# Kernel tuning notes

Hardware: AMD Instinct MI355X
Metric: run time of the kernel (lower is better)

The kernel has to match this reference:

```python
import jax, jax.numpy as jnp
import numpy as np

CHUNK = 128  # chunk size for the chunked causal linear-attention scan
EPS = 1e-6


def _feature_map(x):
    # elu(x) + 1, matching torch.nn.functional.elu (alpha=1)
    return jax.nn.elu(x) + 1.0


def _causal_linear(Q, K, V):
    """Chunked causal linear attention.

    Q, K: [N, H, L, D], V: [N, H, L, Dv] (float32).
    Computes out[l] = Q[l] @ sum_{s<=l} K[s]^T V[s] without materializing
    the O(L*D*Dv) cumulative outer-product tensor.
    """
    N, H, L, D = Q.shape
    Dv = V.shape[-1]
    C = L // CHUNK
    # [C, N, H, T, D]
    qc = jnp.moveaxis(Q.reshape(N, H, C, CHUNK, D), 2, 0)
    kc = jnp.moveaxis(K.reshape(N, H, C, CHUNK, D), 2, 0)
    vc = jnp.moveaxis(V.reshape(N, H, C, CHUNK, Dv), 2, 0)
    tri = jnp.tril(jnp.ones((CHUNK, CHUNK), dtype=Q.dtype))  # causal mask within chunk

    def step(S, qkv):
        q, k, v = qkv  # [N, H, T, D], [N, H, T, D], [N, H, T, Dv]
        attn = jnp.einsum('nhtd,nhsd->nhts', q, k) * tri
        out = jnp.einsum('nhts,nhse->nhte', attn, v) \
            + jnp.einsum('nhtd,nhde->nhte', q, S)
        S = S + jnp.einsum('nhsd,nhse->nhde', k, v)
        return S, out

    S0 = jnp.zeros((N, H, D, Dv), dtype=Q.dtype)
    _, outs = jax.lax.scan(step, S0, (qc, kc, vc))  # outs: [C, N, H, T, Dv]
    return jnp.moveaxis(outs, 0, 2).reshape(N, H, L, Dv)


def setup_inputs() -> dict:
    key = jax.random.key(0)
    kq, kk, kv = jax.random.split(key, 3)
    shape = (4, 8192, 8, 64)  # [N, L, H, D]
    return {
        'queries': jax.random.normal(kq, shape, dtype=jnp.float32),
        'keys': jax.random.normal(kk, shape, dtype=jnp.float32),
        'values': jax.random.normal(kv, shape, dtype=jnp.float32),
    }


def reference(queries, keys, values):
    dtype = queries.dtype
    Q = _feature_map(queries)  # [N, L, H, D]
    K = _feature_map(keys)
    # normalizer: Z = 1 / (Q . cumsum_l(K) + eps), shape [N, L, H]
    Z = 1.0 / (jnp.einsum('nlhi,nlhi->nlh', Q, jnp.cumsum(K, axis=1)) + EPS)
    # numerator computed in float32 per original causal_linear
    Qf = jnp.transpose(Q, (0, 2, 1, 3)).astype(jnp.float32)
    Kf = jnp.transpose(K, (0, 2, 1, 3)).astype(jnp.float32)
    Vf = jnp.transpose(values, (0, 2, 1, 3)).astype(jnp.float32)
    Vn = _causal_linear(Qf, Kf, Vf)  # [N, H, L, Dv]
    Vn = jnp.transpose(Vn, (0, 2, 1, 3)).astype(dtype)  # [N, L, H, Dv]
    return Vn * Z[:, :, :, None]
```

## Files before the change

kernel.cpp:

```cpp
#include <hip/hip_runtime.h>
#include <math.h>

#define N_    4
#define L_    8192
#define H_    8
#define NH_   32
#define CHK   64
#define NC_   128
#define ROWF  512
#define EPSF  1e-6f

typedef __attribute__((ext_vector_type(8))) short bf16x8;
typedef __attribute__((ext_vector_type(4))) float f32x4;
typedef __attribute__((ext_vector_type(4))) unsigned short us4;

__device__ __forceinline__ float fmap(float x) { return x > 0.f ? x + 1.f : __expf(x); }

__device__ __forceinline__ unsigned short f2bf(float x) {
  unsigned u = __float_as_uint(x);
  u += 0x7FFFu + ((u >> 16) & 1u);
  return (unsigned short)(u >> 16);
}
__device__ __forceinline__ float bf2f(unsigned short u) {
  return __uint_as_float(((unsigned)u) << 16);
}

__device__ __forceinline__ int sidx(int row, int col) {
  return row * 64 + (col ^ ((row & 7) << 3));
}

__device__ __forceinline__ f32x4 MFMA(bf16x8 a, bf16x8 b, f32x4 c) {
  return __builtin_amdgcn_mfma_f32_16x16x32_bf16(a, b, c, 0, 0, 0);
}

__global__ __launch_bounds__(256, 4) void k_chunk_tot(const float* __restrict__ keys,
                                                      const float* __restrict__ values,
                                                      unsigned short* __restrict__ Tws,
                                                      float* __restrict__ Kcs) {
  __shared__ __align__(16) unsigned short Kt[64 * 64];
  __shared__ __align__(16) unsigned short Vt[64 * 64];
  __shared__ float kacc[64];
  const int bid = blockIdx.x;
  const int nh = bid / NC_, c = bid % NC_;
  const int n = nh / H_, h = nh % H_;
  const int tid = threadIdx.x;
  const int lane = tid & 63;
  const int wv = tid >> 6;
  const int lane15 = lane & 15, lg = lane >> 4;
  const int arow = wv * 16 + lane15;

  if (tid < 64) kacc[tid] = 0.f;

  const int d = tid & 63, sg = tid >> 6;
  const size_t gbase = ((size_t)(n * L_ + c * CHK)) * ROWF + h * 64 + d;
  float kr[16], vr[16];
#pragma unroll
  for (int i = 0; i < 16; ++i) {
    const size_t g = gbase + (size_t)(sg * 16 + i) * ROWF;
    kr[i] = keys[g];
    vr[i] = values[g];
  }
  float kpart = 0.f;
#pragma unroll
  for (int i = 0; i < 16; i += 4) {
    us4 wk, wvv;
#pragma unroll
    for (int j = 0; j < 4; ++j) {
      const float kf = fmap(kr[i + j]);
      kpart += kf;
      wk[j] = f2bf(kf);
      wvv[j] = f2bf(vr[i + j]);
    }
    *(us4*)&Kt[sidx(d, sg * 16 + i)] = wk;
    *(us4*)&Vt[sidx(d, sg * 16 + i)] = wvv;
  }
  __syncthreads();

  atomicAdd(&kacc[d], kpart);

  const bf16x8 av0 = *(const bf16x8*)&Vt[sidx(arow, lg * 8)];
  const bf16x8 av1 = *(const bf16x8*)&Vt[sidx(arow, (lg + 4) * 8)];
  us4 tf[4];
#pragma unroll
  for (int nt = 0; nt < 4; ++nt) {
    const int brow = nt * 16 + lane15;
    f32x4 acc = {0.f, 0.f, 0.f, 0.f};
    acc = MFMA(*(const bf16x8*)&Kt[sidx(brow, lg * 8)], av0, acc);
    acc = MFMA(*(const bf16x8*)&Kt[sidx(brow, (lg + 4) * 8)], av1, acc);
#pragma unroll
    for (int r = 0; r < 4; ++r) tf[nt][r] = f2bf(acc[r]);
  }
  __syncthreads();

#pragma unroll
  for (int nt = 0; nt < 4; ++nt)
    *(us4*)&Kt[sidx(arow, nt * 16 + lg * 4)] = tf[nt];
  __syncthreads();

  {
    unsigned short* Tp = Tws + (size_t)bid * 4096;
#pragma unroll
    for (int it = 0; it < 2; ++it) {
      const int i8 = (tid + it * 256) * 8;
      *(uint4*)&Tp[i8] = *(const uint4*)&Kt[i8];
    }
  }
  if (tid < 64) Kcs[(size_t)bid * 64 + tid] = kacc[tid];
}

__global__ __launch_bounds__(256) void k_scan(unsigned short* __restrict__ Tws,
                                              float* __restrict__ Kcs) {
  const int tid = threadIdx.x;
  if (blockIdx.x < 512) {
    const int gid = blockIdx.x * 256 + tid;
    const int nh = gid >> 12, de = gid & 4095;
    unsigned short* p = Tws + (size_t)nh * NC_ * 4096 + de;
    float run = 0.f;
    for (int s = 0; s < 32; ++s) {
      const float x0 = bf2f(p[(size_t)(s * 4 + 0) * 4096]);
      const float x1 = bf2f(p[(size_t)(s * 4 + 1) * 4096]);
      const float x2 = bf2f(p[(size_t)(s * 4 + 2) * 4096]);
      const float x3 = bf2f(p[(size_t)(s * 4 + 3) * 4096]);
      p[(size_t)(s * 4 + 0) * 4096] = f2bf(run);
      p[(size_t)(s * 4 + 1) * 4096] = f2bf(run + x0);
      p[(size_t)(s * 4 + 2) * 4096] = f2bf(run + x0 + x1);
      p[(size_t)(s * 4 + 3) * 4096] = f2bf(run + x0 + x1 + x2);
      run += x0 + x1 + x2 + x3;
    }
  } else {
    const int gid = (blockIdx.x - 512) * 256 + tid;
    const int nh = gid >> 6, d = gid & 63;
    float* p = Kcs + (size_t)nh * NC_ * 64 + d;
    float run = 0.f;
    for (int s = 0; s < 32; ++s) {
      const float x0 = p[(size_t)(s * 4 + 0) * 64];
      const float x1 = p[(size_t)(s * 4 + 1) * 64];
      const float x2 = p[(size_t)(s * 4 + 2) * 64];
      const float x3 = p[(size_t)(s * 4 + 3) * 64];
      p[(size_t)(s * 4 + 0) * 64] = run;
      p[(size_t)(s * 4 + 1) * 64] = run + x0;
      p[(size_t)(s * 4 + 2) * 64] = run + x0 + x1;
      p[(size_t)(s * 4 + 3) * 64] = run + x0 + x1 + x2;
      run += x0 + x1 + x2 + x3;
    }
  }
}

__global__ __launch_bounds__(256, 4) void k_output(const float* __restrict__ queries,
                                                   const float* __restrict__ keys,
                                                   const float* __restrict__ values,
                                                   const unsigned short* __restrict__ Pws,
                                                   const float* __restrict__ Kpre,
                                                   float* __restrict__ out) {
  __shared__ __align__(16) unsigned short Ks[64 * 64];
  __shared__ __align__(16) unsigned short Vt[64 * 64];
  __shared__ __align__(16) unsigned short St[64 * 64];
  __shared__ float kpre[64];

  const int wg = blockIdx.x;
  const int bid = (wg & 7) * (NH_ * NC_ / 8) + (wg >> 3);
  const int nh = bid / NC_, c = bid % NC_;
  const int n = nh / H_, h = nh % H_;
  const int tid = threadIdx.x;
  const int lane = tid & 63;
  const int wv = tid >> 6;
  const int lane15 = lane & 15, lg = lane >> 4;
  const int t0w = wv * 16;
  const int trow = t0w + lane15;
  const int l0 = c * CHK;

  const size_t qg = ((size_t)(n * L_ + l0 + trow)) * ROWF + h * 64;
  const float4 q0 = *(const float4*)&queries[qg + lg * 8];
  const float4 q1 = *(const float4*)&queries[qg + lg * 8 + 4];
  const float4 q2 = *(const float4*)&queries[qg + 32 + lg * 8];
  const float4 q3 = *(const float4*)&queries[qg + 32 + lg * 8 + 4];
  const int r0 = tid >> 4, c4 = (tid & 15) * 4;
  float4 kr[4];
#pragma unroll
  for (int rep = 0; rep < 4; ++rep)
    kr[rep] = *(const float4*)&keys[((size_t)(n * L_ + l0 + r0 + rep * 16)) * ROWF + h * 64 + c4];
  const int d = tid & 63, sg = tid >> 6;
  const size_t vbase = ((size_t)(n * L_ + l0)) * ROWF + h * 64 + d;
  float vr[16];
#pragma unroll
  for (int i = 0; i < 16; ++i) vr[i] = values[vbase + (size_t)(sg * 16 + i) * ROWF];
  const size_t tb = (size_t)bid * 4096;
  const uint4 st0 = *(const uint4*)&Pws[tb + tid * 8];
  const uint4 st1 = *(const uint4*)&Pws[tb + (tid + 256) * 8];
  const float kp = (tid < 64) ? Kpre[(size_t)bid * 64 + tid] : 0.f;

  bf16x8 qf0, qf1;
  qf0[0] = (short)f2bf(fmap(q0.x)); qf0[1] = (short)f2bf(fmap(q0.y));
  qf0[2] = (short)f2bf(fmap(q0.z)); qf0[3] = (short)f2bf(fmap(q0.w));
  qf0[4] = (short)f2bf(fmap(q1.x)); qf0[5] = (short)f2bf(fmap(q1.y));
  qf0[6] = (short)f2bf(fmap(q1.z)); qf0[7] = (short)f2bf(fmap(q1.w));
  qf1[0] = (short)f2bf(fmap(q2.x)); qf1[1] = (short)f2bf(fmap(q2.y));
  qf1[2] = (short)f2bf(fmap(q2.z)); qf1[3] = (short)f2bf(fmap(q2.w));
  qf1[4] = (short)f2bf(fmap(q3.x)); qf1[5] = (short)f2bf(fmap(q3.y));
  qf1[6] = (short)f2bf(fmap(q3.z)); qf1[7] = (short)f2bf(fmap(q3.w));
#pragma unroll
  for (int rep = 0; rep < 4; ++rep) {
    us4 uk;
    uk[0] = f2bf(fmap(kr[rep].x)); uk[1] = f2bf(fmap(kr[rep].y));
    uk[2] = f2bf(fmap(kr[rep].z)); uk[3] = f2bf(fmap(kr[rep].w));
    *(us4*)&Ks[sidx(r0 + rep * 16, c4)] = uk;
  }
#pragma unroll
  for (int i = 0; i < 16; i += 4) {
    us4 w;
#pragma unroll
    for (int j = 0; j < 4; ++j) w[j] = f2bf(vr[i + j]);
    *(us4*)&Vt[sidx(d, sg * 16 + i)] = w;
  }
  *(uint4*)&St[tid * 8] = st0;
  *(uint4*)&St[(tid + 256) * 8] = st1;
  if (tid < 64) kpre[tid] = kp;
  __syncthreads();

  f32x4 aT[4];
#pragma unroll
  for (int nt = 0; nt < 4; ++nt) {
    const int srow = nt * 16 + lane15;
    f32x4 a = {0.f, 0.f, 0.f, 0.f};
    a = MFMA(*(const bf16x8*)&Ks[sidx(srow, lg * 8)], qf0, a);
    a = MFMA(*(const bf16x8*)&Ks[sidx(srow, (lg + 4) * 8)], qf1, a);
    aT[nt] = a;
  }
  float zp = 0.f;
#pragma unroll
  for (int j = 0; j < 8; ++j) zp += bf2f((unsigned short)qf0[j]) * kpre[lg * 8 + j];
#pragma unroll
  for (int j = 0; j < 8; ++j) zp += bf2f((unsigned short)qf1[j]) * kpre[32 + lg * 8 + j];

  __syncthreads();

  float rs = 0.f;
#pragma unroll
  for (int nt = 0; nt < 4; ++nt) {
    us4 w;
#pragma unroll
    for (int r = 0; r < 4; ++r) {
      const int s = nt * 16 + lg * 4 + r;
      const float v = (s <= trow) ? aT[nt][r] : 0.f;
      rs += v;
      w[r] = f2bf(v);
    }
    *(us4*)&Ks[sidx(trow, nt * 16 + lg * 4)] = w;
  }
  float den = rs + zp;
  den += __shfl_xor(den, 16);
  den += __shfl_xor(den, 32);
  const float zv = 1.f / (den + EPSF);

  const bf16x8 af0 = *(const bf16x8*)&Ks[sidx(trow, lg * 8)];
  const bf16x8 af1 = *(const bf16x8*)&Ks[sidx(trow, 32 + lg * 8)];
  const size_t obase = ((size_t)(n * L_ + l0 + trow)) * ROWF + h * 64;
#pragma unroll
  for (int nt = 0; nt < 4; ++nt) {
    const int brow = nt * 16 + lane15;
    f32x4 o = {0.f, 0.f, 0.f, 0.f};
    o = MFMA(*(const bf16x8*)&Vt[sidx(brow, lg * 8)], af0, o);
    o = MFMA(*(const bf16x8*)&Vt[sidx(brow, (lg + 4) * 8)], af1, o);
    o = MFMA(*(const bf16x8*)&St[sidx(brow, lg * 8)], qf0, o);
    o = MFMA(*(const bf16x8*)&St[sidx(brow, (lg + 4) * 8)], qf1, o);
    const float4 w = make_float4(o[0] * zv, o[1] * zv, o[2] * zv, o[3] * zv);
    *(float4*)&out[obase + nt * 16 + lg * 4] = w;
  }
}

extern "C" void kernel_launch(void* const* d_in, const int* in_sizes, int n_in,
                              void* d_out, int out_size, void* d_ws, size_t ws_size,
                              hipStream_t stream) {
  const float* queries = (const float*)d_in[0];
  const float* keys    = (const float*)d_in[1];
  const float* values  = (const float*)d_in[2];
  float* out = (float*)d_out;

  const size_t t_elems = (size_t)NH_ * NC_ * 4096;
  const size_t k_elems = (size_t)NH_ * NC_ * 64;
  if (ws_size < t_elems * 2 + k_elems * 4) return;
  unsigned short* Tws = (unsigned short*)d_ws;
  float* Kcs = (float*)(Tws + t_elems);

  hipLaunchKernelGGL(k_chunk_tot, dim3(NH_ * NC_), dim3(256), 0, stream, keys, values, Tws, Kcs);
  hipLaunchKernelGGL(k_scan, dim3(512 + 8), dim3(256), 0, stream, Tws, Kcs);
  hipLaunchKernelGGL(k_output, dim3(NH_ * NC_), dim3(256), 0, stream,
                     queries, keys, values, Tws, Kcs, out);
}
```

Baseline: 92.46 us.

## Stage K/V/state tiles via direct global-to-LDS async loads in both kernels

Replaces per-thread strided scalar global loads of keys/values (and the prefix-state tile) with global_load_lds 16-byte transfers straight into shared memory. Each thread then reads coalesced fp32 rows back from LDS, applies the feature map and bf16 conversion, and transposes into swizzled tiles. The key column sum is now computed from the bf16 tile instead of the fp32 values. The intended gain is fewer uncoalesced global transactions and lower register pressure. In exchange it doubles LDS use to about 32-40 KB per block, drops the occupancy hint from launch_bounds, and adds extra barriers.

Result: slower. 95.34 us (+3.1%).

```diff
diff --git a/kernel.cpp b/kernel.cpp
--- a/kernel.cpp
+++ b/kernel.cpp
@@ -33,13 +33,21 @@
   return __builtin_amdgcn_mfma_f32_16x16x32_bf16(a, b, c, 0, 0, 0);
 }
 
-__global__ __launch_bounds__(256, 4) void k_chunk_tot(const float* __restrict__ keys,
-                                                      const float* __restrict__ values,
-                                                      unsigned short* __restrict__ Tws,
-                                                      float* __restrict__ Kcs) {
-  __shared__ __align__(16) unsigned short Kt[64 * 64];
-  __shared__ __align__(16) unsigned short Vt[64 * 64];
+__device__ __forceinline__ void gload_lds16(const void* g, void* l) {
+  __builtin_amdgcn_global_load_lds(
+      (const __attribute__((address_space(1))) void*)g,
+      (__attribute__((address_space(3))) void*)l, 16, 0, 0);
+}
+
+__global__ __launch_bounds__(256) void k_chunk_tot(const float* __restrict__ keys,
+                                                   const float* __restrict__ values,
+                                                   unsigned short* __restrict__ Tws,
+                                                   float* __restrict__ Kcs) {
+  __shared__ __align__(16) float Raw[8192];
   __shared__ float kacc[64];
+  unsigned short* Kt = (unsigned short*)Raw;
+  unsigned short* Vt = (unsigned short*)(Raw + 4096);
+  unsigned short* Tt = (unsigned short*)(Raw + 6144);
   const int bid = blockIdx.x;
   const int nh = bid / NC_, c = bid % NC_;
   const int n = nh / H_, h = nh % H_;
@@ -51,32 +59,49 @@
 
   if (tid < 64) kacc[tid] = 0.f;
 
-  const int d = tid & 63, sg = tid >> 6;
-  const size_t gbase = ((size_t)(n * L_ + c * CHK)) * ROWF + h * 64 + d;
-  float kr[16], vr[16];
-#pragma unroll
-  for (int i = 0; i < 16; ++i) {
-    const size_t g = gbase + (size_t)(sg * 16 + i) * ROWF;
-    kr[i] = keys[g];
-    vr[i] = values[g];
-  }
-  float kpart = 0.f;
-#pragma unroll
-  for (int i = 0; i < 16; i += 4) {
-    us4 wk, wvv;
+  {
+    const size_t rowbase = (size_t)(n * L_ + c * CHK);
+    const size_t coff = (size_t)h * 64 + (lane & 15) * 4;
+#pragma unroll
+    for (int b = 0; b < 4; ++b) {
+      const int s4 = wv * 16 + b * 4;
+      const size_t g = (rowbase + s4 + (lane >> 4)) * ROWF + coff;
+      gload_lds16(&keys[g],   &Raw[s4 * 64]);
+      gload_lds16(&values[g], &Raw[4096 + s4 * 64]);
+    }
+  }
+  __syncthreads();
+
+  const int s = tid >> 2, dg = tid & 3;
+  f32x4 kq[4], vq[4];
+#pragma unroll
+  for (int q = 0; q < 4; ++q) {
+    kq[q] = *(const f32x4*)&Raw[s * 64 + dg * 16 + q * 4];
+    vq[q] = *(const f32x4*)&Raw[4096 + s * 64 + dg * 16 + q * 4];
+  }
+  __syncthreads();
+#pragma unroll
+  for (int q = 0; q < 4; ++q) {
 #pragma unroll
     for (int j = 0; j < 4; ++j) {
-      const float kf = fmap(kr[i + j]);
-      kpart += kf;
-      wk[j] = f2bf(kf);
-      wvv[j] = f2bf(vr[i + j]);
-    }
-    *(us4*)&Kt[sidx(d, sg * 16 + i)] = wk;
-    *(us4*)&Vt[sidx(d, sg * 16 + i)] = wvv;
-  }
-  __syncthreads();
-
-  atomicAdd(&kacc[d], kpart);
+      const int dd = dg * 16 + q * 4 + j;
+      Kt[sidx(dd, s)] = f2bf(fmap(kq[q][j]));
+      Vt[sidx(dd, s)] = f2bf(vq[q][j]);
+    }
+  }
+  __syncthreads();
+
+  {
+    const int d2 = tid & 63, sg2 = tid >> 6;
+    float ksum = 0.f;
+#pragma unroll
+    for (int i4 = 0; i4 < 4; ++i4) {
+      const us4 w = *(const us4*)&Kt[sidx(d2, sg2 * 16 + i4 * 4)];
+#pragma unroll
+      for (int j = 0; j < 4; ++j) ksum += bf2f(w[j]);
+    }
+    atomicAdd(&kacc[d2], ksum);
+  }
 
   const bf16x8 av0 = *(const bf16x8*)&Vt[sidx(arow, lg * 8)];
   const bf16x8 av1 = *(const bf16x8*)&Vt[sidx(arow, (lg + 4) * 8)];
@@ -90,11 +115,9 @@
 #pragma unroll
     for (int r = 0; r < 4; ++r) tf[nt][r] = f2bf(acc[r]);
   }
-  __syncthreads();
-
 #pragma unroll
   for (int nt = 0; nt < 4; ++nt)
-    *(us4*)&Kt[sidx(arow, nt * 16 + lg * 4)] = tf[nt];
+    *(us4*)&Tt[sidx(arow, nt * 16 + lg * 4)] = tf[nt];
   __syncthreads();
 
   {
@@ -102,7 +125,7 @@
 #pragma unroll
     for (int it = 0; it < 2; ++it) {
       const int i8 = (tid + it * 256) * 8;
-      *(uint4*)&Tp[i8] = *(const uint4*)&Kt[i8];
+      *(uint4*)&Tp[i8] = *(const uint4*)&Tt[i8];
     }
   }
   if (tid < 64) Kcs[(size_t)bid * 64 + tid] = kacc[tid];
@@ -146,16 +169,17 @@
   }
 }
 
-__global__ __launch_bounds__(256, 4) void k_output(const float* __restrict__ queries,
-                                                   const float* __restrict__ keys,
-                                                   const float* __restrict__ values,
-                                                   const unsigned short* __restrict__ Pws,
-                                                   const float* __restrict__ Kpre,
-                                                   float* __restrict__ out) {
-  __shared__ __align__(16) unsigned short Ks[64 * 64];
-  __shared__ __align__(16) unsigned short Vt[64 * 64];
-  __shared__ __align__(16) unsigned short St[64 * 64];
+__global__ __launch_bounds__(256) void k_output(const float* __restrict__ queries,
+                                                const float* __restrict__ keys,
+                                                const float* __restrict__ values,
+                                                const unsigned short* __restrict__ Pws,
+                                                const float* __restrict__ Kpre,
+                                                float* __restrict__ out) {
+  __shared__ __align__(16) float Raw[8192];
+  __shared__ __align__(16) unsigned short St[4096];
   __shared__ float kpre[64];
+  unsigned short* Ks = (unsigned short*)Raw;
+  unsigned short* Vt = (unsigned short*)(Raw + 4096);
 
   const int wg = blockIdx.x;
   const int bid = (wg & 7) * (NH_ * NC_ / 8) + (wg >> 3);
@@ -168,27 +192,50 @@
   const int t0w = wv * 16;
   const int trow = t0w + lane15;
   const int l0 = c * CHK;
-
+  const size_t tb = (size_t)bid * 4096;
+
+  {
+    const size_t rowbase = (size_t)(n * L_ + l0);
+    const size_t coff = (size_t)h * 64 + (lane & 15) * 4;
+#pragma unroll
+    for (int b = 0; b < 4; ++b) {
+      const int s4 = wv * 16 + b * 4;
+      const size_t g = (rowbase + s4 + (lane >> 4)) * ROWF + coff;
+      gload_lds16(&keys[g],   &Raw[s4 * 64]);
+      gload_lds16(&values[g], &Raw[4096 + s4 * 64]);
+    }
+#pragma unroll
+    for (int b = 0; b < 2; ++b) {
+      const int u0 = wv * 1024 + b * 512;
+      gload_lds16(&Pws[tb + u0 + lane * 8], &St[u0]);
+    }
+  }
   const size_t qg = ((size_t)(n * L_ + l0 + trow)) * ROWF + h * 64;
   const float4 q0 = *(const float4*)&queries[qg + lg * 8];
   const float4 q1 = *(const float4*)&queries[qg + lg * 8 + 4];
   const float4 q2 = *(const float4*)&queries[qg + 32 + lg * 8];
   const float4 q3 = *(const float4*)&queries[qg + 32 + lg * 8 + 4];
-  const int r0 = tid >> 4, c4 = (tid & 15) * 4;
-  float4 kr[4];
-#pragma unroll
-  for (int rep = 0; rep < 4; ++rep)
-    kr[rep] = *(const float4*)&keys[((size_t)(n * L_ + l0 + r0 + rep * 16)) * ROWF + h * 64 + c4];
-  const int d = tid & 63, sg = tid >> 6;
-  const size_t vbase = ((size_t)(n * L_ + l0)) * ROWF + h * 64 + d;
-  float vr[16];
-#pragma unroll
-  for (int i = 0; i < 16; ++i) vr[i] = values[vbase + (size_t)(sg * 16 + i) * ROWF];
-  const size_t tb = (size_t)bid * 4096;
-  const uint4 st0 = *(const uint4*)&Pws[tb + tid * 8];
-  const uint4 st1 = *(const uint4*)&Pws[tb + (tid + 256) * 8];
   const float kp = (tid < 64) ? Kpre[(size_t)bid * 64 + tid] : 0.f;
-
+  __syncthreads();
+
+  const int s = tid >> 2, dg = tid & 3;
+  f32x4 kq[4], vq[4];
+#pragma unroll
+  for (int q = 0; q < 4; ++q) {
+    kq[q] = *(const f32x4*)&Raw[s * 64 + dg * 16 + q * 4];
+    vq[q] = *(const f32x4*)&Raw[4096 + s * 64 + dg * 16 + q * 4];
+  }
+  __syncthreads();
+#pragma unroll
+  for (int q = 0; q < 4; ++q) {
+    us4 wk;
+#pragma unroll
+    for (int j = 0; j < 4; ++j) {
+      wk[j] = f2bf(fmap(kq[q][j]));
+      Vt[sidx(dg * 16 + q * 4 + j, s)] = f2bf(vq[q][j]);
+    }
+    *(us4*)&Ks[sidx(s, dg * 16 + q * 4)] = wk;
+  }
   bf16x8 qf0, qf1;
   qf0[0] = (short)f2bf(fmap(q0.x)); qf0[1] = (short)f2bf(fmap(q0.y));
   qf0[2] = (short)f2bf(fmap(q0.z)); qf0[3] = (short)f2bf(fmap(q0.w));
@@ -198,22 +245,6 @@
   qf1[2] = (short)f2bf(fmap(q2.z)); qf1[3] = (short)f2bf(fmap(q2.w));
   qf1[4] = (short)f2bf(fmap(q3.x)); qf1[5] = (short)f2bf(fmap(q3.y));
   qf1[6] = (short)f2bf(fmap(q3.z)); qf1[7] = (short)f2bf(fmap(q3.w));
-#pragma unroll
-  for (int rep = 0; rep < 4; ++rep) {
-    us4 uk;
-    uk[0] = f2bf(fmap(kr[rep].x)); uk[1] = f2bf(fmap(kr[rep].y));
-    uk[2] = f2bf(fmap(kr[rep].z)); uk[3] = f2bf(fmap(kr[rep].w));
-    *(us4*)&Ks[sidx(r0 + rep * 16, c4)] = uk;
-  }
-#pragma unroll
-  for (int i = 0; i < 16; i += 4) {
-    us4 w;
-#pragma unroll
-    for (int j = 0; j < 4; ++j) w[j] = f2bf(vr[i + j]);
-    *(us4*)&Vt[sidx(d, sg * 16 + i)] = w;
-  }
-  *(uint4*)&St[tid * 8] = st0;
-  *(uint4*)&St[(tid + 256) * 8] = st1;
   if (tid < 64) kpre[tid] = kp;
   __syncthreads();
 
@@ -240,8 +271,8 @@
     us4 w;
 #pragma unroll
     for (int r = 0; r < 4; ++r) {
-      const int s = nt * 16 + lg * 4 + r;
-      const float v = (s <= trow) ? aT[nt][r] : 0.f;
+      const int sc = nt * 16 + lg * 4 + r;
+      const float v = (sc <= trow) ? aT[nt][r] : 0.f;
       rs += v;
       w[r] = f2bf(v);
     }
```
